# Kernel tuning notes

Hardware: AMD Instinct MI355X
Metric: run time of the kernel (lower is better)

Reference implementation:

```python
import jax, jax.numpy as jnp
import numpy as np

D_K = 1024
NHEADS = 16
HEAD_DIM = D_K // NHEADS  # 64
STD = float(np.sqrt(HEAD_DIM))  # matches math.sqrt(d_k // nheads)


def setup_inputs() -> dict:
    key = jax.random.key(0)
    ks = jax.random.split(key, 9)
    B, S = 2, 2048
    scale = 1.0 / np.sqrt(D_K)
    x = jax.random.normal(ks[0], (B, S, D_K), dtype=jnp.float32)
    Wq = jax.random.normal(ks[1], (D_K, D_K), dtype=jnp.float32) * scale
    bq = jnp.zeros((D_K,), dtype=jnp.float32)
    Wk = jax.random.normal(ks[2], (D_K, D_K), dtype=jnp.float32) * scale
    bk = jnp.zeros((D_K,), dtype=jnp.float32)
    Wv = jax.random.normal(ks[3], (D_K, D_K), dtype=jnp.float32) * scale
    bv = jnp.zeros((D_K,), dtype=jnp.float32)
    Wo = jax.random.normal(ks[4], (D_K, D_K), dtype=jnp.float32) * scale
    bo = jnp.zeros((D_K,), dtype=jnp.float32)
    return {"x": x, "Wq": Wq, "bq": bq, "Wk": Wk, "bk": bk,
            "Wv": Wv, "bv": bv, "Wo": Wo, "bo": bo}


def _heads(x, W, b):
    # Linear then split heads: (B,S,D) -> (B,H,S,hd)
    B, S, _ = x.shape
    out = x @ W.T + b
    return out.reshape(B, S, NHEADS, HEAD_DIM).transpose(0, 2, 1, 3)


def reference(x, Wq, bq, Wk, bk, Wv, bv, Wo, bo):
    B, S, _ = x.shape
    q = _heads(x, Wq, bq)  # (B,H,S,hd)
    k = _heads(x, Wk, bk)
    v = _heads(x, Wv, bv)
    scores = jnp.einsum('bhqd,bhkd->bhqk', q, k) / STD  # (B,H,S,S)
    causal = jnp.tril(jnp.ones((S, S), dtype=bool))  # mask_factory default
    scores = jnp.where(causal[None, None, :, :], scores, -jnp.inf)
    attn = jax.nn.softmax(scores, axis=-1)
    ctx = jnp.einsum('bhqk,bhkd->bhqd', attn, v)  # (B,H,S,hd)
    ctx = ctx.transpose(0, 2, 1, 3).reshape(B, S, D_K)
    return ctx @ Wo.T + bo
```

## Files before the change

### kernel.cpp

```cpp
#include <hip/hip_runtime.h>
#include <stdint.h>

typedef unsigned short u16;
typedef __bf16 bf16x8 __attribute__((ext_vector_type(8)));
typedef __bf16 bf16x4v __attribute__((ext_vector_type(4)));
typedef float f32x4 __attribute__((ext_vector_type(4)));

typedef __attribute__((address_space(3))) uint32_t lds_u32;
typedef __attribute__((address_space(1))) uint32_t glb_u32;

__device__ __forceinline__ f32x4 mfma16(bf16x8 a, bf16x8 b, f32x4 c) {
    return __builtin_amdgcn_mfma_f32_16x16x32_bf16(a, b, c, 0, 0, 0);
}

__device__ __forceinline__ ushort4 pk4(float a, float b, float c, float d) {
    bf16x4v v;
    v[0] = (__bf16)a; v[1] = (__bf16)b; v[2] = (__bf16)c; v[3] = (__bf16)d;
    union { bf16x4v v; ushort4 u; } cv; cv.v = v; return cv.u;
}

__device__ __forceinline__ void async16(const u16* g, u16* l) {
    __builtin_amdgcn_global_load_lds((glb_u32*)(uintptr_t)(const void*)g,
                                     (lds_u32*)l, 16, 0, 0);
}

__global__ __launch_bounds__(256) void cast_all(
    const float* __restrict__ x,
    const float* __restrict__ w0, const float* __restrict__ w1,
    const float* __restrict__ w2, const float* __restrict__ w3,
    u16* __restrict__ xo, u16* __restrict__ o0, u16* __restrict__ o1,
    u16* __restrict__ o2, u16* __restrict__ o3)
{
    const int s = blockIdx.y;
    const int i = (blockIdx.x * 256 + threadIdx.x) * 4;
    if (s == 0) {
#pragma unroll
        for (int c = 0; c < 4; ++c) {
            const int j = i + c * (1 << 20);
            float4 v = *(const float4*)(x + j);
            *(ushort4*)(xo + j) = pk4(v.x, v.y, v.z, v.w);
        }
    } else {
        const float* in = s == 1 ? w0 : (s == 2 ? w1 : (s == 3 ? w2 : w3));
        u16* out       = s == 1 ? o0 : (s == 2 ? o1 : (s == 3 ? o2 : o3));
        float4 v = *(const float4*)(in + i);
        *(ushort4*)(out + i) = pk4(v.x, v.y, v.z, v.w);
    }
}

__global__ __launch_bounds__(256) void gemm_qkv(
    const u16* __restrict__ A,
    const u16* __restrict__ W0, const u16* __restrict__ W1, const u16* __restrict__ W2,
    const float* __restrict__ B0, const float* __restrict__ B1, const float* __restrict__ B2,
    u16* __restrict__ O0, u16* __restrict__ O1,
    u16* __restrict__ VT,
    int M, int N, int K)
{
    const int x = blockIdx.x & 7;
    const int L = blockIdx.x >> 3;
    const int tm = (8 * (x >> 1) + (L & 7)) << 7;
    const int tnsel = 12 * (x & 1) + (L >> 3);
    const int sel = tnsel >> 3;
    const int tn  = (tnsel & 7) << 7;

    const u16* W      = sel == 0 ? W0 : (sel == 1 ? W1 : W2);
    const float* bias = sel == 0 ? B0 : (sel == 1 ? B1 : B2);
    u16* O            = sel == 0 ? O0 : O1;

    __shared__ __attribute__((aligned(16))) u16 As[128 * 64];
    __shared__ __attribute__((aligned(16))) u16 Bs[128 * 64];
    u16 (*Tb)[136] = (u16 (*)[136])As;

    const int tid  = threadIdx.x;
    const int lane = tid & 63;
    const int w    = tid >> 6;
    const int l15  = lane & 15;
    const int quad = lane >> 4;

    const int wm = (w >> 1) << 6;
    const int wn = (w & 1) << 6;

    f32x4 acc[4][4];
#pragma unroll
    for (int i = 0; i < 4; ++i)
#pragma unroll
        for (int j = 0; j < 4; ++j) acc[i][j] = f32x4{0.f, 0.f, 0.f, 0.f};

    const int lr  = lane >> 3;
    const int lcc = lane & 7;
    const int scc = lcc ^ lr;
    const u16* Ag = A + (size_t)(tm + 32 * w + lr) * K + scc * 8;
    const u16* Wg = W + (size_t)(tn + 32 * w + lr) * K + scc * 8;
    u16* Al = &As[(32 * w + lr) * 64 + lcc * 8];
    u16* Bl = &Bs[(32 * w + lr) * 64 + lcc * 8];

    for (int k0 = 0; k0 < K; k0 += 64) {
        __syncthreads();
#pragma unroll
        for (int m = 0; m < 4; ++m) {
            async16(Ag + k0 + (size_t)m * 8 * K, Al + m * 512);
            async16(Wg + k0 + (size_t)m * 8 * K, Bl + m * 512);
        }
        asm volatile("s_waitcnt vmcnt(0)" ::: "memory");
        __syncthreads();

#pragma unroll
        for (int kk = 0; kk < 2; ++kk) {
            bf16x8 a[4], b[4];
#pragma unroll
            for (int i = 0; i < 4; ++i) {
                const int r  = wm + 16 * i + l15;
                const int sl = (kk * 4 + quad) ^ (r & 7);
                a[i] = *(const bf16x8*)&As[r * 64 + sl * 8];
            }
#pragma unroll
            for (int j = 0; j < 4; ++j) {
                const int r  = wn + 16 * j + l15;
                const int sl = (kk * 4 + quad) ^ (r & 7);
                b[j] = *(const bf16x8*)&Bs[r * 64 + sl * 8];
            }
#pragma unroll
            for (int i = 0; i < 4; ++i)
#pragma unroll
                for (int j = 0; j < 4; ++j)
                    acc[i][j] = mfma16(a[i], b[j], acc[i][j]);
        }
    }

    if (sel == 2) {
        const int bb = tm >> 11;
        const int s0 = tm & 2047;
        const size_t vtb = ((size_t)bb << 10) + tn;
        for (int c32 = 0; c32 < 128; c32 += 32) {
            __syncthreads();
            if ((c32 >> 6) == (wn >> 6)) {
                const int j0 = (c32 >> 4) & 2;
#pragma unroll
                for (int jj = 0; jj < 2; ++jj) {
                    const int j  = j0 + jj;
                    const int cc = jj * 16 + l15;
                    const float bj = bias[tn + wn + 16 * j + l15];
#pragma unroll
                    for (int i = 0; i < 4; ++i) {
                        const int rr = wm + 16 * i + quad * 4;
                        *(ushort4*)&Tb[cc][rr] =
                            pk4(acc[i][j][0] + bj, acc[i][j][1] + bj,
                                acc[i][j][2] + bj, acc[i][j][3] + bj);
                    }
                }
            }
            __syncthreads();
            {
                const int c  = tid >> 3;
                const int ss = (tid & 7) * 16;
                uint4 v0 = *(const uint4*)&Tb[c][ss];
                uint4 v1 = *(const uint4*)&Tb[c][ss + 8];
                u16* dst = &VT[(vtb + c32 + c) * 2048 + s0 + ss];
                *(uint4*)dst       = v0;
                *(uint4*)(dst + 8) = v1;
            }
        }
    } else {
#pragma unroll
        for (int j = 0; j < 4; ++j) {
            const int col = tn + wn + 16 * j + l15;
            const float bj = bias[col];
#pragma unroll
            for (int i = 0; i < 4; ++i) {
                const int row = tm + wm + 16 * i + quad * 4;
#pragma unroll
                for (int r = 0; r < 4; ++r) {
                    union { float f; unsigned u; } v; v.f = acc[i][j][r] + bj;
                    unsigned rn = v.u + 0x7FFFu + ((v.u >> 16) & 1u);
                    O[(size_t)(row + r) * N + col] = (u16)(rn >> 16);
                }
            }
        }
    }
}

__global__ __launch_bounds__(256) void gemm_out64(
    const u16* __restrict__ A, const u16* __restrict__ W,
    const float* __restrict__ bias, float* __restrict__ O,
    int M, int N, int K)
{
    __shared__ __attribute__((aligned(16))) u16 As[128 * 64];
    __shared__ __attribute__((aligned(16))) u16 Bs[64 * 64];

    const int x = blockIdx.x & 7;
    const int L = blockIdx.x >> 3;
    const int tm = (8 * (x >> 1) + (L & 7)) << 7;
    const int tn = (8 * (x & 1) + (L >> 3)) << 6;

    const int tid  = threadIdx.x;
    const int lane = tid & 63;
    const int w    = tid >> 6;
    const int l15  = lane & 15;
    const int quad = lane >> 4;

    const int wm = (w >> 1) << 6;
    const int wn = (w & 1) << 5;

    f32x4 acc[4][2];
#pragma unroll
    for (int i = 0; i < 4; ++i)
#pragma unroll
        for (int j = 0; j < 2; ++j) acc[i][j] = f32x4{0.f, 0.f, 0.f, 0.f};

    const int lr  = lane >> 3;
    const int lcc = lane & 7;
    const int scc = lcc ^ lr;
    const u16* Ag = A + (size_t)(tm + 32 * w + lr) * K + scc * 8;
    const u16* Wg = W + (size_t)(tn + 16 * w + lr) * K + scc * 8;
    u16* Al = &As[(32 * w + lr) * 64 + lcc * 8];
    u16* Bl = &Bs[(16 * w + lr) * 64 + lcc * 8];

    for (int k0 = 0; k0 < K; k0 += 64) {
        __syncthreads();
#pragma unroll
        for (int m = 0; m < 4; ++m)
            async16(Ag + k0 + (size_t)m * 8 * K, Al + m * 512);
#pragma unroll
        for (int m = 0; m < 2; ++m)
            async16(Wg + k0 + (size_t)m * 8 * K, Bl + m * 512);
        asm volatile("s_waitcnt vmcnt(0)" ::: "memory");
        __syncthreads();

#pragma unroll
        for (int kk = 0; kk < 2; ++kk) {
            bf16x8 a[4], b[2];
#pragma unroll
            for (int i = 0; i < 4; ++i) {
                const int r  = wm + 16 * i + l15;
                const int sl = (kk * 4 + quad) ^ (r & 7);
                a[i] = *(const bf16x8*)&As[r * 64 + sl * 8];
            }
#pragma unroll
            for (int j = 0; j < 2; ++j) {
                const int r  = wn + 16 * j + l15;
                const int sl = (kk * 4 + quad) ^ (r & 7);
                b[j] = *(const bf16x8*)&Bs[r * 64 + sl * 8];
            }
#pragma unroll
            for (int i = 0; i < 4; ++i)
#pragma unroll
                for (int j = 0; j < 2; ++j)
                    acc[i][j] = mfma16(a[i], b[j], acc[i][j]);
        }
    }

#pragma unroll
    for (int j = 0; j < 2; ++j) {
        const int col = tn + wn + 16 * j + l15;
        const float bj = bias[col];
#pragma unroll
        for (int i = 0; i < 4; ++i) {
            const int row = tm + wm + 16 * i + quad * 4;
#pragma unroll
            for (int r = 0; r < 4; ++r)
                O[(size_t)(row + r) * N + col] = acc[i][j][r] + bj;
        }
    }
}

__device__ __forceinline__ bf16x8 rdt(const u16* base, int t, int l15, int cc) {
    const int r = t * 16 + l15;
    const int c = (cc & 3) ^ (r & 3);
    return *(const bf16x8*)(base + (cc >> 2) * 2048 + r * 32 + c * 8);
}

__global__ __launch_bounds__(256) void attn6(
    const u16* __restrict__ Q, const u16* __restrict__ Kb,
    const u16* __restrict__ VT, u16* __restrict__ ctx)
{
    __shared__ __attribute__((aligned(16))) u16 Kt[2][4096];
    __shared__ __attribute__((aligned(16))) u16 Vt[2][4096];
    __shared__ __attribute__((aligned(16))) u16 Pt[4][32][72];

    const int tid  = threadIdx.x;
    const int lane = tid & 63;
    const int wid  = tid >> 6;
    const int l15  = lane & 15;
    const int quad = lane >> 4;

    const int hb = blockIdx.x & 31;
    const int h  = hb & 15, b = hb >> 4;
    const int ti = blockIdx.x >> 5;
    const int g  = (ti & 1) ? (15 - (ti >> 1)) : (ti >> 1);

    const int sL = 4 * g + wid, sH = 127 - sL;
    const int KL = g, KH = 31 - g;

    const size_t rowbase = (size_t)b * 2048;
    const int cbase = h * 64;
    const u16* kbase = Kb + rowbase * 1024 + cbase;
    const u16* vbase = VT + ((size_t)b * 1024 + cbase) * 2048;

    const int qgL = sL * 16 + l15, qgH = sH * 16 + l15;
    const u16* qpL = Q + (rowbase + qgL) * 1024 + cbase + quad * 8;
    const u16* qpH = Q + (rowbase + qgH) * 1024 + cbase + quad * 8;
    const bf16x8 qL0 = *(const bf16x8*)qpL, qL1 = *(const bf16x8*)(qpL + 32);
    const bf16x8 qH0 = *(const bf16x8*)qpH, qH1 = *(const bf16x8*)(qpH + 32);

    const int sr  = tid >> 2;
    const int sc0 = (((tid & 3) ^ (sr & 3)) << 3);
    const u16* kg = kbase + (size_t)sr * 1024 + sc0;
    const u16* vg = vbase + (size_t)sr * 2048 + sc0;

    f32x4 oL[4], oH[4];
#pragma unroll
    for (int i = 0; i < 4; ++i) { oL[i] = f32x4{0,0,0,0}; oH[i] = f32x4{0,0,0,0}; }
    float rsL = 0.f, rsH = 0.f;
    const float SC = 0.18033688011112042f;

    u16 (*ptw)[72] = Pt[wid];

    async16(kg,      &Kt[0][tid * 8]);
    async16(kg + 32, &Kt[0][2048 + tid * 8]);
    async16(vg,      &Vt[0][tid * 8]);
    async16(vg + 32, &Vt[0][2048 + tid * 8]);

    for (int kt = 0; kt <= KH; ++kt) {
        const int cur = kt & 1, nxt = cur ^ 1;
        asm volatile("s_waitcnt vmcnt(0)" ::: "memory");
        __syncthreads();
        if (kt < KH) {
            const u16* kgn = kg + (size_t)(kt + 1) * 65536;
            const u16* vgn = vg + (kt + 1) * 64;
            async16(kgn,      &Kt[nxt][tid * 8]);
            async16(kgn + 32, &Kt[nxt][2048 + tid * 8]);
            async16(vgn,      &Vt[nxt][tid * 8]);
            async16(vgn + 32, &Vt[nxt][2048 + tid * 8]);
        }
        const u16* KT = Kt[cur];
        const u16* VL = Vt[cur];
        const bool doL = (kt <= KL);
        const bool mH = (kt == KH), mL = (kt == KL);

        float pH[4][4], pL[4][4];
#pragma unroll
        for (int t = 0; t < 4; ++t) {
            const bf16x8 kA = rdt(KT, t, l15, quad);
            const bf16x8 kB = rdt(KT, t, l15, quad + 4);
            f32x4 zH = {0,0,0,0};
            zH = mfma16(kA, qH0, zH);
            zH = mfma16(kB, qH1, zH);
            f32x4 zL = {0,0,0,0};
            if (doL) {
                zL = mfma16(kA, qL0, zL);
                zL = mfma16(kB, qL1, zL);
            }
#pragma unroll
            for (int r = 0; r < 4; ++r) {
                float v = fmaf(zH[r], SC, -16.0f);
                if (mH && (kt * 64 + t * 16 + quad * 4 + r) > qgH) v = -1e30f;
                const float e = exp2f(v);
                pH[t][r] = e; rsH += e;
                if (doL) {
                    float vl = fmaf(zL[r], SC, -16.0f);
                    if (mL && (kt * 64 + t * 16 + quad * 4 + r) > qgL) vl = -1e30f;
                    const float el = exp2f(vl);
                    pL[t][r] = el; rsL += el;
                }
            }
        }

#pragma unroll
        for (int t = 0; t < 4; ++t)
            *(ushort4*)&ptw[16 + l15][t * 16 + quad * 4] =
                pk4(pH[t][0], pH[t][1], pH[t][2], pH[t][3]);
        if (doL) {
#pragma unroll
            for (int t = 0; t < 4; ++t)
                *(ushort4*)&ptw[l15][t * 16 + quad * 4] =
                    pk4(pL[t][0], pL[t][1], pL[t][2], pL[t][3]);
        }

        const bf16x8 bH0 = *(const bf16x8*)&ptw[16 + l15][quad * 8];
        const bf16x8 bH1 = *(const bf16x8*)&ptw[16 + l15][32 + quad * 8];
#pragma unroll
        for (int t = 0; t < 4; ++t) {
            const bf16x8 vA = rdt(VL, t, l15, quad);
            const bf16x8 vB = rdt(VL, t, l15, quad + 4);
            oH[t] = mfma16(vA, bH0, oH[t]);
            oH[t] = mfma16(vB, bH1, oH[t]);
        }
        if (doL) {
            const bf16x8 bL0 = *(const bf16x8*)&ptw[l15][quad * 8];
            const bf16x8 bL1 = *(const bf16x8*)&ptw[l15][32 + quad * 8];
#pragma unroll
            for (int t = 0; t < 4; ++t) {
                const bf16x8 vA = rdt(VL, t, l15, quad);
                const bf16x8 vB = rdt(VL, t, l15, quad + 4);
                oL[t] = mfma16(vA, bL0, oL[t]);
                oL[t] = mfma16(vB, bL1, oL[t]);
            }
        }
    }

    rsH += __shfl_xor(rsH, 16); rsH += __shfl_xor(rsH, 32);
    rsL += __shfl_xor(rsL, 16); rsL += __shfl_xor(rsL, 32);
    const float iH = 1.0f / rsH, iL = 1.0f / rsL;
#pragma unroll
    for (int t = 0; t < 4; ++t) {
        *(ushort4*)&ctx[(rowbase + qgL) * 1024 + cbase + t * 16 + quad * 4] =
            pk4(oL[t][0] * iL, oL[t][1] * iL, oL[t][2] * iL, oL[t][3] * iL);
        *(ushort4*)&ctx[(rowbase + qgH) * 1024 + cbase + t * 16 + quad * 4] =
            pk4(oH[t][0] * iH, oH[t][1] * iH, oH[t][2] * iH, oH[t][3] * iH);
    }
}

extern "C" void kernel_launch(void* const* d_in, const int* in_sizes, int n_in,
                              void* d_out, int out_size, void* d_ws, size_t ws_size,
                              hipStream_t stream) {
    const float* x  = (const float*)d_in[0];
    const float* Wq = (const float*)d_in[1];
    const float* bq = (const float*)d_in[2];
    const float* Wk = (const float*)d_in[3];
    const float* bk = (const float*)d_in[4];
    const float* Wv = (const float*)d_in[5];
    const float* bv = (const float*)d_in[6];
    const float* Wo = (const float*)d_in[7];
    const float* bo = (const float*)d_in[8];
    float* out = (float*)d_out;

    const int N = 1024, K = 1024;
    const int M = in_sizes[0] / K;
    const size_t MN = (size_t)M * N;
    const size_t WN = (size_t)N * K;

    u16* xb  = (u16*)d_ws;
    u16* wqb = xb  + MN;
    u16* wkb = wqb + WN;
    u16* wvb = wkb + WN;
    u16* wob = wvb + WN;
    u16* q   = wob + WN;
    u16* kb  = q   + MN;
    u16* vt  = kb  + MN;
    u16* ctx = q;

    cast_all<<<dim3(1024, 5), 256, 0, stream>>>(
        x, Wq, Wk, Wv, Wo, xb, wqb, wkb, wvb, wob);

    gemm_qkv<<<dim3(768), 256, 0, stream>>>(
        xb, wqb, wkb, wvb, bq, bk, bv, q, kb, vt, M, N, K);

    attn6<<<dim3(512), 256, 0, stream>>>(q, kb, vt, ctx);

    gemm_out64<<<dim3(512), 256, 0, stream>>>(
        ctx, wob, bo, out, M, N, K);
}
```

Measured before the change: 202.1 us.

## Restructure attention inner loop with swizzled LDS, raw exp2, and MFMA priority

After: 194.6 us. 1.04x faster.

```diff
diff --git a/kernel.cpp b/kernel.cpp
--- a/kernel.cpp
+++ b/kernel.cpp
@@ -17,6 +17,10 @@
     bf16x4v v;
     v[0] = (__bf16)a; v[1] = (__bf16)b; v[2] = (__bf16)c; v[3] = (__bf16)d;
     union { bf16x4v v; ushort4 u; } cv; cv.v = v; return cv.u;
+}
+
+__device__ __forceinline__ float fexp2(float x) {
+    return __builtin_amdgcn_exp2f(x);
 }
 
 __device__ __forceinline__ void async16(const u16* g, u16* l) {
@@ -265,23 +269,48 @@
 
 __device__ __forceinline__ bf16x8 rdt(const u16* base, int t, int l15, int cc) {
     const int r = t * 16 + l15;
-    const int c = (cc & 3) ^ (r & 3);
+    const int c = (cc & 3) ^ ((r >> 1) & 3);
     return *(const bf16x8*)(base + (cc >> 2) * 2048 + r * 32 + c * 8);
 }
 
-__global__ __launch_bounds__(256) void attn6(
+#define QK_EXP(Z, PROW, QG, MASKED, RSV, KB)                                   \
+    do {                                                                       \
+        _Pragma("unroll")                                                      \
+        for (int t = 0; t < 4; ++t) {                                          \
+            float e0 = fexp2(fmaf((Z)[t][0], SC, -16.0f));                     \
+            float e1 = fexp2(fmaf((Z)[t][1], SC, -16.0f));                     \
+            float e2 = fexp2(fmaf((Z)[t][2], SC, -16.0f));                     \
+            float e3 = fexp2(fmaf((Z)[t][3], SC, -16.0f));                     \
+            if (MASKED) {                                                      \
+                const int kb = (KB) + t * 16 + quad * 4;                       \
+                if (kb + 0 > (QG)) e0 = 0.f;                                   \
+                if (kb + 1 > (QG)) e1 = 0.f;                                   \
+                if (kb + 2 > (QG)) e2 = 0.f;                                   \
+                if (kb + 3 > (QG)) e3 = 0.f;                                   \
+            }                                                                  \
+            (RSV)[0] += e0; (RSV)[1] += e1;                                    \
+            (RSV)[2] += e2; (RSV)[3] += e3;                                    \
+            *(ushort4*)((PROW) + (((2 * t + whi) ^ sl7) << 3) + woff) =        \
+                pk4(e0, e1, e2, e3);                                           \
+        }                                                                      \
+    } while (0)
+
+__global__ __launch_bounds__(256) void attn7(
     const u16* __restrict__ Q, const u16* __restrict__ Kb,
     const u16* __restrict__ VT, u16* __restrict__ ctx)
 {
     __shared__ __attribute__((aligned(16))) u16 Kt[2][4096];
     __shared__ __attribute__((aligned(16))) u16 Vt[2][4096];
-    __shared__ __attribute__((aligned(16))) u16 Pt[4][32][72];
+    __shared__ __attribute__((aligned(16))) u16 Pt[4][32][64];
 
     const int tid  = threadIdx.x;
     const int lane = tid & 63;
     const int wid  = tid >> 6;
     const int l15  = lane & 15;
     const int quad = lane >> 4;
+    const int sl7  = l15 & 7;
+    const int whi  = quad >> 1;
+    const int woff = (quad & 1) * 4;
 
     const int hb = blockIdx.x & 31;
     const int h  = hb & 15, b = hb >> 4;
@@ -303,17 +332,19 @@
     const bf16x8 qH0 = *(const bf16x8*)qpH, qH1 = *(const bf16x8*)(qpH + 32);
 
     const int sr  = tid >> 2;
-    const int sc0 = (((tid & 3) ^ (sr & 3)) << 3);
+    const int sc0 = (((tid & 3) ^ ((sr >> 1) & 3)) << 3);
     const u16* kg = kbase + (size_t)sr * 1024 + sc0;
     const u16* vg = vbase + (size_t)sr * 2048 + sc0;
 
     f32x4 oL[4], oH[4];
 #pragma unroll
     for (int i = 0; i < 4; ++i) { oL[i] = f32x4{0,0,0,0}; oH[i] = f32x4{0,0,0,0}; }
-    float rsL = 0.f, rsH = 0.f;
+    f32x4 rsLv = {0,0,0,0}, rsHv = {0,0,0,0};
     const float SC = 0.18033688011112042f;
 
-    u16 (*ptw)[72] = Pt[wid];
+    u16 (*ptw)[64] = Pt[wid];
+    u16* const prH = &ptw[16 + l15][0];
+    u16* const prL = &ptw[l15][0];
 
     async16(kg,      &Kt[0][tid * 8]);
     async16(kg + 32, &Kt[0][2048 + tid * 8]);
@@ -337,67 +368,74 @@
         const bool doL = (kt <= KL);
         const bool mH = (kt == KH), mL = (kt == KL);
 
-        float pH[4][4], pL[4][4];
-#pragma unroll
-        for (int t = 0; t < 4; ++t) {
-            const bf16x8 kA = rdt(KT, t, l15, quad);
-            const bf16x8 kB = rdt(KT, t, l15, quad + 4);
-            f32x4 zH = {0,0,0,0};
-            zH = mfma16(kA, qH0, zH);
-            zH = mfma16(kB, qH1, zH);
-            f32x4 zL = {0,0,0,0};
-            if (doL) {
-                zL = mfma16(kA, qL0, zL);
-                zL = mfma16(kB, qL1, zL);
-            }
-#pragma unroll
-            for (int r = 0; r < 4; ++r) {
-                float v = fmaf(zH[r], SC, -16.0f);
-                if (mH && (kt * 64 + t * 16 + quad * 4 + r) > qgH) v = -1e30f;
-                const float e = exp2f(v);
-                pH[t][r] = e; rsH += e;
-                if (doL) {
-                    float vl = fmaf(zL[r], SC, -16.0f);
-                    if (mL && (kt * 64 + t * 16 + quad * 4 + r) > qgL) vl = -1e30f;
-                    const float el = exp2f(vl);
-                    pL[t][r] = el; rsL += el;
-                }
-            }
-        }
-
-#pragma unroll
-        for (int t = 0; t < 4; ++t)
-            *(ushort4*)&ptw[16 + l15][t * 16 + quad * 4] =
-                pk4(pH[t][0], pH[t][1], pH[t][2], pH[t][3]);
+        f32x4 zH[4], zL[4];
+        __builtin_amdgcn_s_setprio(1);
         if (doL) {
 #pragma unroll
-            for (int t = 0; t < 4; ++t)
-                *(ushort4*)&ptw[l15][t * 16 + quad * 4] =
-                    pk4(pL[t][0], pL[t][1], pL[t][2], pL[t][3]);
-        }
-
-        const bf16x8 bH0 = *(const bf16x8*)&ptw[16 + l15][quad * 8];
-        const bf16x8 bH1 = *(const bf16x8*)&ptw[16 + l15][32 + quad * 8];
-#pragma unroll
-        for (int t = 0; t < 4; ++t) {
-            const bf16x8 vA = rdt(VL, t, l15, quad);
-            const bf16x8 vB = rdt(VL, t, l15, quad + 4);
-            oH[t] = mfma16(vA, bH0, oH[t]);
-            oH[t] = mfma16(vB, bH1, oH[t]);
-        }
+            for (int t = 0; t < 4; ++t) {
+                const bf16x8 kA = rdt(KT, t, l15, quad);
+                const bf16x8 kB = rdt(KT, t, l15, quad + 4);
+                f32x4 zh = {0,0,0,0};
+                zh = mfma16(kA, qH0, zh);
+                zh = mfma16(kB, qH1, zh);
+                zH[t] = zh;
+                f32x4 zl = {0,0,0,0};
+                zl = mfma16(kA, qL0, zl);
+                zl = mfma16(kB, qL1, zl);
+                zL[t] = zl;
+            }
+        } else {
+#pragma unroll
+            for (int t = 0; t < 4; ++t) {
+                const bf16x8 kA = rdt(KT, t, l15, quad);
+                const bf16x8 kB = rdt(KT, t, l15, quad + 4);
+                f32x4 zh = {0,0,0,0};
+                zh = mfma16(kA, qH0, zh);
+                zh = mfma16(kB, qH1, zh);
+                zH[t] = zh;
+            }
+        }
+        __builtin_amdgcn_s_setprio(0);
+
+        const int ktb = kt * 64;
+        if (mH) QK_EXP(zH, prH, qgH, 1, rsHv, ktb);
+        else    QK_EXP(zH, prH, qgH, 0, rsHv, ktb);
         if (doL) {
-            const bf16x8 bL0 = *(const bf16x8*)&ptw[l15][quad * 8];
-            const bf16x8 bL1 = *(const bf16x8*)&ptw[l15][32 + quad * 8];
+            if (mL) QK_EXP(zL, prL, qgL, 1, rsLv, ktb);
+            else    QK_EXP(zL, prL, qgL, 0, rsLv, ktb);
+        }
+
+        const bf16x8 bH0 = *(const bf16x8*)(prH + ((quad ^ sl7) << 3));
+        const bf16x8 bH1 = *(const bf16x8*)(prH + (((quad | 4) ^ sl7) << 3));
+        if (doL) {
+            const bf16x8 bL0 = *(const bf16x8*)(prL + ((quad ^ sl7) << 3));
+            const bf16x8 bL1 = *(const bf16x8*)(prL + (((quad | 4) ^ sl7) << 3));
+            __builtin_amdgcn_s_setprio(1);
 #pragma unroll
             for (int t = 0; t < 4; ++t) {
                 const bf16x8 vA = rdt(VL, t, l15, quad);
                 const bf16x8 vB = rdt(VL, t, l15, quad + 4);
+                oH[t] = mfma16(vA, bH0, oH[t]);
+                oH[t] = mfma16(vB, bH1, oH[t]);
                 oL[t] = mfma16(vA, bL0, oL[t]);
                 oL[t] = mfma16(vB, bL1, oL[t]);
             }
-        }
-    }
-
+            __builtin_amdgcn_s_setprio(0);
+        } else {
+            __builtin_amdgcn_s_setprio(1);
+#pragma unroll
+            for (int t = 0; t < 4; ++t) {
+                const bf16x8 vA = rdt(VL, t, l15, quad);
+                const bf16x8 vB = rdt(VL, t, l15, quad + 4);
+                oH[t] = mfma16(vA, bH0, oH[t]);
+                oH[t] = mfma16(vB, bH1, oH[t]);
+            }
+            __builtin_amdgcn_s_setprio(0);
+        }
+    }
+
+    float rsH = (rsHv[0] + rsHv[1]) + (rsHv[2] + rsHv[3]);
+    float rsL = (rsLv[0] + rsLv[1]) + (rsLv[2] + rsLv[3]);
     rsH += __shfl_xor(rsH, 16); rsH += __shfl_xor(rsH, 32);
     rsL += __shfl_xor(rsL, 16); rsL += __shfl_xor(rsL, 32);
     const float iH = 1.0f / rsH, iL = 1.0f / rsL;
@@ -445,7 +483,7 @@
     gemm_qkv<<<dim3(768), 256, 0, stream>>>(
         xb, wqb, wkb, wvb, bq, bk, bv, q, kb, vt, M, N, K);
 
-    attn6<<<dim3(512), 256, 0, stream>>>(q, kb, vt, ctx);
+    attn7<<<dim3(512), 256, 0, stream>>>(q, kb, vt, ctx);
 
     gemm_out64<<<dim3(512), 256, 0, stream>>>(
         ctx, wob, bo, out, M, N, K);
```
